# Optimization experiments

Hardware: AMD Instinct MI355X
Metric: run time of the kernel (lower is better)

## Reference

```python
import jax, jax.numpy as jnp
import numpy as np

EPS = 1e-08


def _norm(H, add):
    # Faithful to GTN.norm: transpose, mask/set diagonal, row-normalize by degree, transpose back.
    # The original O(N^3) mm(deg_inv_diag, H) is expressed as an O(N^2) row scaling (same math).
    Ht = H.T
    n = Ht.shape[0]
    eye = jnp.eye(n, dtype=H.dtype)
    Ht = Ht * (1.0 - eye)
    if add:
        Ht = Ht + eye
    deg = jnp.sum(Ht, axis=1)
    deg_inv = jnp.where(deg == 0, 0.0, 1.0 / (deg + EPS))
    return (deg_inv[:, None] * Ht).T


def _gtconv(A, w):
    # A: [E, N, N]; w: [C, E, 1, 1] -> softmax over E, weighted sum of adjacency channels.
    s = jax.nn.softmax(w[:, :, 0, 0], axis=1)  # [C, E]
    return jnp.einsum('ce,eij->cij', s, A)     # [C, N, N]


def setup_inputs() -> dict:
    key = jax.random.key(0)
    k = jax.random.split(key, 6)
    E, N, C, w_in, w_out = 5, 2048, 2, 256, 64
    A = jax.random.uniform(k[0], (E, N, N), dtype=jnp.float32)
    X = jax.random.normal(k[1], (N, w_in), dtype=jnp.float32)
    conv_w_l0_1 = jax.random.normal(k[2], (C, E, 1, 1), dtype=jnp.float32)
    conv_w_l0_2 = jax.random.normal(k[3], (C, E, 1, 1), dtype=jnp.float32)
    conv_w_l1 = jax.random.normal(k[4], (C, E, 1, 1), dtype=jnp.float32)
    gcn_weight = jax.random.normal(k[5], (w_in, w_out), dtype=jnp.float32) * (1.0 / np.sqrt(w_in))
    return {"A": A, "X": X, "conv_w_l0_1": conv_w_l0_1, "conv_w_l0_2": conv_w_l0_2,
            "conv_w_l1": conv_w_l1, "gcn_weight": gcn_weight}


def reference(A, X, conv_w_l0_1, conv_w_l0_2, conv_w_l1, gcn_weight):
    N = A.shape[1]
    # Layer 0 (first=True): two GTConvs, meta-path composition via bmm.
    a = _gtconv(A, conv_w_l0_1)            # [C, N, N]
    b = _gtconv(A, conv_w_l0_2)            # [C, N, N]
    H = jnp.einsum('cij,cjk->cik', a, b)   # [C, N, N]
    # Layer 1 (first=False): normalize per channel, then compose with new conv.
    H = jax.vmap(lambda h: _norm(h, False))(H)
    a1 = _gtconv(A, conv_w_l1)
    H = jnp.einsum('cij,cjk->cik', H, a1)
    # GCN readout per channel: mm(norm_add(H_c).T, X @ W), relu, concat along features.
    Xw = X @ gcn_weight                     # [N, w_out]
    Hn = jax.vmap(lambda h: _norm(h, True))(H)   # [C, N, N]
    Xc = jax.nn.relu(jnp.einsum('cji,jk->cik', Hn, Xw))  # [C, N, w_out]
    X_ = jnp.transpose(Xc, (1, 0, 2)).reshape(N, -1)     # [N, C*w_out]
    return X_
```

## Files before the change

kernel.cpp:

```cpp
#include <hip/hip_runtime.h>
#include <cstdint>
#include <cstddef>

typedef unsigned short u16;
typedef __attribute__((ext_vector_type(8))) short short8;
typedef __attribute__((ext_vector_type(4))) float v4f;

static constexpr size_t NN = (size_t)2048 * 2048;
#define N2 2048

typedef __attribute__((address_space(1))) const unsigned int guint;
typedef __attribute__((address_space(3))) unsigned int luint;

__device__ __forceinline__ float b2f_bits(uint32_t hi) { union { uint32_t u; float f; } v; v.u = hi; return v.f; }
__device__ __forceinline__ float b2f(u16 x) { return b2f_bits((uint32_t)x << 16); }
__device__ __forceinline__ u16 f2b(float f) {
  union { float f; uint32_t u; } v; v.f = f;
  uint32_t r = v.u + 0x7fffu + ((v.u >> 16) & 1u);
  return (u16)(r >> 16);
}
__device__ __forceinline__ uint4 pack8(const float* f) {
  uint4 u;
  u.x = (uint32_t)f2b(f[0]) | ((uint32_t)f2b(f[1]) << 16);
  u.y = (uint32_t)f2b(f[2]) | ((uint32_t)f2b(f[3]) << 16);
  u.z = (uint32_t)f2b(f[4]) | ((uint32_t)f2b(f[5]) << 16);
  u.w = (uint32_t)f2b(f[6]) | ((uint32_t)f2b(f[7]) << 16);
  return u;
}
__device__ __forceinline__ void unp8(uint4 u, float* f) {
  f[0] = b2f_bits(u.x << 16); f[1] = b2f_bits(u.x & 0xffff0000u);
  f[2] = b2f_bits(u.y << 16); f[3] = b2f_bits(u.y & 0xffff0000u);
  f[4] = b2f_bits(u.z << 16); f[5] = b2f_bits(u.z & 0xffff0000u);
  f[6] = b2f_bits(u.w << 16); f[7] = b2f_bits(u.w & 0xffff0000u);
}
__device__ __forceinline__ float sgprf(float x) {
  union { float f; int i; } v; v.f = x;
  v.i = __builtin_amdgcn_readfirstlane(v.i);
  return v.f;
}

__global__ __launch_bounds__(512, 2) void conv_kernel(
    const float* __restrict__ A, const float* __restrict__ w1,
    const float* __restrict__ w2, const float* __restrict__ w3,
    const float* __restrict__ X, const float* __restrict__ W,
    u16* __restrict__ abf, u16* __restrict__ bbt, u16* __restrict__ a1t,
    u16* __restrict__ a1r, u16* __restrict__ Xwt)
{
  __shared__ u16 LT[4][64 * 64];
  const int t = threadIdx.x;
  const int i0 = blockIdx.y * 64, j0 = blockIdx.x * 64;
  const int m = t >> 3;
  const int cg = t & 7;
  const int n0 = cg * 8;

  float sc[3][2][5];
  {
    const float* wsrc[3] = { w1, w2, w3 };
    for (int q = 0; q < 3; ++q)
      for (int c = 0; c < 2; ++c) {
        float v[5], mx = -1e30f, sum = 0.f;
        #pragma unroll
        for (int e = 0; e < 5; ++e) { v[e] = wsrc[q][c * 5 + e]; mx = fmaxf(mx, v[e]); }
        #pragma unroll
        for (int e = 0; e < 5; ++e) { v[e] = expf(v[e] - mx); sum += v[e]; }
        #pragma unroll
        for (int e = 0; e < 5; ++e) sc[q][c][e] = sgprf(v[e] / sum);
      }
  }

  float av[2][8], bv[2][8], cv[2][8];
  #pragma unroll
  for (int c = 0; c < 2; ++c)
    #pragma unroll
    for (int u = 0; u < 8; ++u) { av[c][u] = 0.f; bv[c][u] = 0.f; cv[c][u] = 0.f; }

  #pragma unroll
  for (int e = 0; e < 5; ++e) {
    const float* base = A + (size_t)e * NN + (size_t)(i0 + m) * N2 + (j0 + n0);
    float4 x0 = ((const float4*)base)[0];
    float4 x1 = ((const float4*)base)[1];
    float f[8] = { x0.x, x0.y, x0.z, x0.w, x1.x, x1.y, x1.z, x1.w };
    #pragma unroll
    for (int c = 0; c < 2; ++c)
      #pragma unroll
      for (int u = 0; u < 8; ++u) {
        av[c][u] += sc[0][c][e] * f[u];
        bv[c][u] += sc[1][c][e] * f[u];
        cv[c][u] += sc[2][c][e] * f[u];
      }
  }

  #pragma unroll
  for (int c = 0; c < 2; ++c) {
    *(uint4*)(abf + (size_t)c * NN + (size_t)(i0 + m) * N2 + (j0 + n0)) = pack8(av[c]);
    *(uint4*)(a1r + (size_t)c * NN + (size_t)(i0 + m) * N2 + (j0 + n0)) = pack8(cv[c]);
  }
  const int swb = ((m >> 3) ^ cg) & 7;
  const int mlo = m & 7;
  #pragma unroll
  for (int c = 0; c < 2; ++c)
    #pragma unroll
    for (int u = 0; u < 8; ++u) {
      const int idx = (n0 + u) * 64 + swb * 8 + mlo;
      LT[c][idx]     = f2b(bv[c][u]);
      LT[2 + c][idx] = f2b(cv[c][u]);
    }
  __syncthreads();
  {
    const int on = t >> 3;
    const int mb = t & 7;
    const int src = on * 64 + (((mb ^ (on >> 3)) & 7) * 8);
    #pragma unroll
    for (int c = 0; c < 2; ++c) {
      *(uint4*)(bbt + (size_t)c * NN + (size_t)(j0 + on) * N2 + (i0 + mb * 8)) =
          *(const uint4*)&LT[c][src];
      *(uint4*)(a1t + (size_t)c * NN + (size_t)(j0 + on) * N2 + (i0 + mb * 8)) =
          *(const uint4*)&LT[2 + c][src];
    }
  }
  if (blockIdx.y < 8) {
    const int n = (int)(blockIdx.y * 32 + blockIdx.x) * 8 + (t >> 6);
    const int k = t & 63;
    float acc = 0.f;
    for (int mm = 0; mm < 256; ++mm)
      acc += X[n * 256 + mm] * W[mm * 64 + k];
    Xwt[(size_t)k * N2 + n] = f2b(acc);
  }
}

template<bool TOUT>
__global__ __launch_bounds__(256, 3) void gemm_kernel(
    const u16* __restrict__ Ain, const u16* __restrict__ Btin,
    u16* __restrict__ Cout, float* __restrict__ csp, float* __restrict__ diag)
{
  const int c = blockIdx.z;
  const u16* Ac = Ain + (size_t)c * NN;
  const u16* Bc = Btin + (size_t)c * NN;
  const int m0 = blockIdx.y * 128, n0 = blockIdx.x * 128;
  const int t = threadIdx.x, w = t >> 6, lane = t & 63;
  const int quad = lane >> 4, r = lane & 15;
  __shared__ u16 SM[128 * 64 + 128 * 64];
  u16* As = SM;
  u16* Bs = SM + 128 * 64;

  v4f zero4 = { 0.f, 0.f, 0.f, 0.f };
  v4f acc[2][8];
  #pragma unroll
  for (int i = 0; i < 2; ++i)
    #pragma unroll
    for (int j = 0; j < 8; ++j) acc[i][j] = zero4;

  const int srow = lane >> 3;
  const int sgran = (lane & 7) ^ srow;

  for (int kt = 0; kt < 2048; kt += 64) {
    __syncthreads();
    #pragma unroll
    for (int i = 0; i < 4; ++i) {
      const int chunk = i * 4 + w;
      const u16* ga = Ac + (size_t)(m0 + chunk * 8 + srow) * N2 + kt + sgran * 8;
      __builtin_amdgcn_global_load_lds((guint*)ga, (luint*)(As + chunk * 512), 16, 0, 0);
    }
    #pragma unroll
    for (int i = 0; i < 4; ++i) {
      const int chunk = i * 4 + w;
      const u16* gb = Bc + (size_t)(n0 + chunk * 8 + srow) * N2 + kt + sgran * 8;
      __builtin_amdgcn_global_load_lds((guint*)gb, (luint*)(Bs + chunk * 512), 16, 0, 0);
    }
    __syncthreads();
    #pragma unroll
    for (int ks = 0; ks < 2; ++ks) {
      const int sl = ((ks * 4 + quad) ^ (r & 7)) * 8;
      short8 af[2], bf[8];
      #pragma unroll
      for (int i = 0; i < 2; ++i)
        af[i] = *(const short8*)(As + (w * 32 + i * 16 + r) * 64 + sl);
      #pragma unroll
      for (int j = 0; j < 8; ++j)
        bf[j] = *(const short8*)(Bs + (j * 16 + r) * 64 + sl);
      #pragma unroll
      for (int i = 0; i < 2; ++i)
        #pragma unroll
        for (int j = 0; j < 8; ++j)
          acc[i][j] = __builtin_amdgcn_mfma_f32_16x16x32_bf16(af[i], bf[j], acc[i][j], 0, 0, 0);
    }
  }
  if (blockIdx.x == blockIdx.y) {
    #pragma unroll
    for (int i = 0; i < 2; ++i) {
      const int rowg = m0 + w * 32 + i * 16 + quad * 4;
      #pragma unroll
      for (int j = 0; j < 8; ++j) {
        const int colg = n0 + j * 16 + r;
        #pragma unroll
        for (int g = 0; g < 4; ++g)
          if (rowg + g == colg) diag[c * N2 + colg] = acc[i][j][g];
      }
    }
  }
  if constexpr (!TOUT) {
    u16* Cc = Cout + (size_t)c * NN;
    #pragma unroll
    for (int i = 0; i < 2; ++i) {
      const int rowg = m0 + w * 32 + i * 16 + quad * 4;
      #pragma unroll
      for (int j = 0; j < 8; ++j) {
        const int colg = n0 + j * 16 + r;
        #pragma unroll
        for (int g = 0; g < 4; ++g)
          Cc[(size_t)(rowg + g) * N2 + colg] = f2b(acc[i][j][g]);
      }
    }
  }
  float s[8];
  #pragma unroll
  for (int j = 0; j < 8; ++j) {
    s[j] = 0.f;
    #pragma unroll
    for (int i = 0; i < 2; ++i)
      #pragma unroll
      for (int g = 0; g < 4; ++g) s[j] += acc[i][j][g];
    s[j] += __shfl_xor(s[j], 16);
    s[j] += __shfl_xor(s[j], 32);
  }
  __syncthreads();
  float* csl = (float*)SM;
  if (quad == 0) {
    #pragma unroll
    for (int j = 0; j < 8; ++j) csl[w * 128 + j * 16 + r] = s[j];
  }
  __syncthreads();
  if (t < 128) {
    const float v = csl[t] + csl[128 + t] + csl[256 + t] + csl[384 + t];
    csp[((size_t)(c * 16) + blockIdx.y) * N2 + n0 + t] = v;
  }
  if constexpr (TOUT) {
    u16* tb = SM;
    u16* Cc = Cout + (size_t)c * NN;
    #pragma unroll
    for (int h = 0; h < 2; ++h) {
      __syncthreads();
      #pragma unroll
      for (int i = 0; i < 2; ++i) {
        #pragma unroll
        for (int jl = 0; jl < 4; ++jl) {
          const int j = h * 4 + jl;
          #pragma unroll
          for (int g = 0; g < 4; ++g)
            tb[(jl * 16 + r) * 136 + (w * 32 + i * 16 + quad * 4 + g)] = f2b(acc[i][j][g]);
        }
      }
      __syncthreads();
      const int rown = t >> 2, seg = t & 3;
      const u16* ps = tb + rown * 136 + seg * 32;
      uint4* pd = (uint4*)(Cc + (size_t)(n0 + h * 64 + rown) * N2 + m0 + seg * 32);
      pd[0] = ((const uint4*)ps)[0];
      pd[1] = ((const uint4*)ps)[1];
      pd[2] = ((const uint4*)ps)[2];
      pd[3] = ((const uint4*)ps)[3];
    }
  }
}

__global__ __launch_bounds__(256) void zgemm_kernel(
    const u16* __restrict__ Ht, const u16* __restrict__ Xwt, float* __restrict__ Zp,
    const float* __restrict__ csp, const float* __restrict__ diag,
    float* __restrict__ ci, float* __restrict__ wv)
{
  const int c = blockIdx.z, split = blockIdx.y;
  const int m0 = blockIdx.x * 128;
  const u16* Ac = Ht + (size_t)c * NN;
  const int t = threadIdx.x, w = t >> 6, lane = t & 63;
  const int quad = lane >> 4, r = lane & 15;
  __shared__ u16 As[128 * 64];
  __shared__ u16 Bs[64 * 64];

  v4f zero4 = { 0.f, 0.f, 0.f, 0.f };
  v4f acc[2][4];
  #pragma unroll
  for (int i = 0; i < 2; ++i)
    #pragma unroll
    for (int j = 0; j < 4; ++j) acc[i][j] = zero4;

  const int srow = lane >> 3;
  const int sgran = (lane & 7) ^ srow;

  for (int kk = 0; kk < 4; ++kk) {
    const int kt = split * 256 + kk * 64;
    __syncthreads();
    #pragma unroll
    for (int i = 0; i < 4; ++i) {
      const int chunk = i * 4 + w;
      const u16* ga = Ac + (size_t)(m0 + chunk * 8 + srow) * N2 + kt + sgran * 8;
      __builtin_amdgcn_global_load_lds((guint*)ga, (luint*)(As + chunk * 512), 16, 0, 0);
    }
    #pragma unroll
    for (int i = 0; i < 2; ++i) {
      const int chunk = i * 4 + w;
      const u16* gb = Xwt + (size_t)(chunk * 8 + srow) * N2 + kt + sgran * 8;
      __builtin_amdgcn_global_load_lds((guint*)gb, (luint*)(Bs + chunk * 512), 16, 0, 0);
    }
    __syncthreads();
    #pragma unroll
    for (int ks = 0; ks < 2; ++ks) {
      const int sl = ((ks * 4 + quad) ^ (r & 7)) * 8;
      short8 af[2], bf[4];
      #pragma unroll
      for (int i = 0; i < 2; ++i)
        af[i] = *(const short8*)(As + (w * 32 + i * 16 + r) * 64 + sl);
      #pragma unroll
      for (int j = 0; j < 4; ++j)
        bf[j] = *(const short8*)(Bs + (j * 16 + r) * 64 + sl);
      #pragma unroll
      for (int i = 0; i < 2; ++i)
        #pragma unroll
        for (int j = 0; j < 4; ++j)
          acc[i][j] = __builtin_amdgcn_mfma_f32_16x16x32_bf16(af[i], bf[j], acc[i][j], 0, 0, 0);
    }
  }
  const size_t pbase = (size_t)(split * 2 + c) * 64;
  #pragma unroll
  for (int i = 0; i < 2; ++i) {
    const int rowg = m0 + w * 32 + i * 16 + quad * 4;
    #pragma unroll
    for (int j = 0; j < 4; ++j) {
      const int colg = j * 16 + r;
      *(v4f*)(Zp + (pbase + colg) * (size_t)N2 + rowg) = acc[i][j];
    }
  }
  if (blockIdx.x == 0 && blockIdx.y == 0) {
    for (int q = t; q < 2048; q += 256) {
      float cs = 0.f;
      #pragma unroll
      for (int s = 0; s < 16; ++s) cs += csp[((size_t)(c * 16) + s) * N2 + q];
      const float deg = cs - diag[c * N2 + q];
      const float v = (deg == 0.f) ? 0.f : 1.f / (deg + 1e-8f);
      ci[c * N2 + q] = v;
      wv[c * N2 + q] = v * deg;
    }
  }
}

__global__ __launch_bounds__(256) void dcol_kernel(
    const u16* __restrict__ Ht, const u16* __restrict__ a1r,
    const float* __restrict__ ci, const float* __restrict__ wv,
    float* __restrict__ dp, float* __restrict__ cp)
{
  const int qg = blockIdx.x, c = blockIdx.y;
  const int p0 = threadIdx.x * 8;
  float dacc[8] = {0,0,0,0,0,0,0,0};
  float cacc[8] = {0,0,0,0,0,0,0,0};
  const u16* hb = Ht  + (size_t)c * NN + (size_t)(qg * 16) * N2 + p0;
  const u16* ab = a1r + (size_t)c * NN + (size_t)(qg * 16) * N2 + p0;
  for (int qq = 0; qq < 16; ++qq) {
    const int q = qg * 16 + qq;
    const float cq = ci[c * N2 + q];
    const float wq = wv[c * N2 + q];
    uint4 hu = *(const uint4*)(hb + (size_t)qq * N2);
    uint4 au = *(const uint4*)(ab + (size_t)qq * N2);
    float h[8], a[8];
    unp8(hu, h); unp8(au, a);
    #pragma unroll
    for (int u = 0; u < 8; ++u) {
      cacc[u] += wq * a[u];
      const float tv = cq * h[u] * a[u];
      dacc[u] += (p0 + u == q) ? 0.f : tv;
    }
  }
  float* dd = dp + (size_t)(c * 128 + qg) * N2 + p0;
  float* cd = cp + (size_t)(c * 128 + qg) * N2 + p0;
  v4f d0 = { dacc[0], dacc[1], dacc[2], dacc[3] };
  v4f d1 = { dacc[4], dacc[5], dacc[6], dacc[7] };
  v4f c0 = { cacc[0], cacc[1], cacc[2], cacc[3] };
  v4f c1 = { cacc[4], cacc[5], cacc[6], cacc[7] };
  *(v4f*)dd = d0; *(v4f*)(dd + 4) = d1;
  *(v4f*)cd = c0; *(v4f*)(cd + 4) = c1;
}

__global__ __launch_bounds__(256) void yfix_kernel(
    const float* __restrict__ Zp, const float* __restrict__ ci,
    const float* __restrict__ diag1, const u16* __restrict__ Xwt,
    u16* __restrict__ Yt)
{
  const int idx = blockIdx.x * 256 + threadIdx.x;
  const int i = idx & 2047, k = (idx >> 11) & 63, c = idx >> 17;
  float z = 0.f;
  #pragma unroll
  for (int s = 0; s < 8; ++s)
    z += Zp[(size_t)((s * 2 + c) * 64 + k) * N2 + i];
  const float xw = b2f(Xwt[(size_t)k * N2 + i]);
  const float y = ci[c * N2 + i] * (z - diag1[c * N2 + i] * xw);
  Yt[(size_t)c * 64 * N2 + (size_t)k * N2 + i] = f2b(y);
}

__global__ void fin_kernel(const float* __restrict__ dp, const float* __restrict__ cp,
                           float* __restrict__ diag2, float* __restrict__ dinv2)
{
  const int idx = blockIdx.x * 256 + threadIdx.x;
  const int c = idx >> 11, i = idx & 2047;
  float ds = 0.f, cs = 0.f;
  for (int b = 0; b < 128; ++b) {
    ds += dp[(size_t)(c * 128 + b) * N2 + i];
    cs += cp[(size_t)(c * 128 + b) * N2 + i];
  }
  const float deg = cs - ds + 1.0f;
  diag2[idx] = ds;
  dinv2[idx] = (deg == 0.f) ? 0.f : 1.f / (deg + 1e-8f);
}

__global__ __launch_bounds__(256) void tgemm_kernel(
    const u16* __restrict__ a1t, const u16* __restrict__ Yt, float* __restrict__ Tp)
{
  const int c = blockIdx.z, split = blockIdx.y;
  const int m0 = blockIdx.x * 128;
  const u16* Ac = a1t + (size_t)c * NN;
  const u16* Bc = Yt + (size_t)c * (64 * (size_t)N2);
  const int t = threadIdx.x, w = t >> 6, lane = t & 63;
  const int quad = lane >> 4, r = lane & 15;
  __shared__ u16 As[128 * 64];
  __shared__ u16 Bs[64 * 64];

  v4f zero4 = { 0.f, 0.f, 0.f, 0.f };
  v4f acc[2][4];
  #pragma unroll
  for (int i = 0; i < 2; ++i)
    #pragma unroll
    for (int j = 0; j < 4; ++j) acc[i][j] = zero4;

  const int srow = lane >> 3;
  const int sgran = (lane & 7) ^ srow;

  for (int kk = 0; kk < 4; ++kk) {
    const int kt = split * 256 + kk * 64;
    __syncthreads();
    #pragma unroll
    for (int i = 0; i < 4; ++i) {
      const int chunk = i * 4 + w;
      const u16* ga = Ac + (size_t)(m0 + chunk * 8 + srow) * N2 + kt + sgran * 8;
      __builtin_amdgcn_global_load_lds((guint*)ga, (luint*)(As + chunk * 512), 16, 0, 0);
    }
    #pragma unroll
    for (int i = 0; i < 2; ++i) {
      const int chunk = i * 4 + w;
      const u16* gb = Bc + (size_t)(chunk * 8 + srow) * N2 + kt + sgran * 8;
      __builtin_amdgcn_global_load_lds((guint*)gb, (luint*)(Bs + chunk * 512), 16, 0, 0);
    }
    __syncthreads();
    #pragma unroll
    for (int ks = 0; ks < 2; ++ks) {
      const int sl = ((ks * 4 + quad) ^ (r & 7)) * 8;
      short8 af[2], bf[4];
      #pragma unroll
      for (int i = 0; i < 2; ++i)
        af[i] = *(const short8*)(As + (w * 32 + i * 16 + r) * 64 + sl);
      #pragma unroll
      for (int j = 0; j < 4; ++j)
        bf[j] = *(const short8*)(Bs + (j * 16 + r) * 64 + sl);
      #pragma unroll
      for (int i = 0; i < 2; ++i)
        #pragma unroll
        for (int j = 0; j < 4; ++j)
          acc[i][j] = __builtin_amdgcn_mfma_f32_16x16x32_bf16(af[i], bf[j], acc[i][j], 0, 0, 0);
    }
  }
  const size_t pbase = (size_t)(split * 2 + c) * 2048;
  #pragma unroll
  for (int i = 0; i < 2; ++i) {
    const int rowg = m0 + w * 32 + i * 16 + quad * 4;
    #pragma unroll
    for (int j = 0; j < 4; ++j) {
      const int colg = j * 16 + r;
      #pragma unroll
      for (int g = 0; g < 4; ++g)
        Tp[(pbase + rowg + g) * 64 + colg] = acc[i][j][g];
    }
  }
}

__global__ void epilogue_kernel(const float* __restrict__ Tp, const float* __restrict__ diag2,
                                const float* __restrict__ dinv2, const u16* __restrict__ Xwt,
                                float* __restrict__ out)
{
  const int idx = blockIdx.x * 256 + threadIdx.x;
  const int k = idx & 63;
  const int c = (idx >> 6) & 1;
  const int i = idx >> 7;
  float T = 0.f;
  #pragma unroll
  for (int s = 0; s < 8; ++s)
    T += Tp[((size_t)(s * 2 + c) * 2048 + i) * 64 + k];
  const float hd = diag2[c * N2 + i];
  const float dv = dinv2[c * N2 + i];
  const float xw = b2f(Xwt[(size_t)k * N2 + i]);
  float v = dv * (T - hd * xw + xw);
  v = v > 0.f ? v : 0.f;
  out[(size_t)i * 128 + c * 64 + k] = v;
}

extern "C" void kernel_launch(void* const* d_in, const int* in_sizes, int n_in,
                              void* d_out, int out_size, void* d_ws, size_t ws_size,
                              hipStream_t stream) {
  const float* A  = (const float*)d_in[0];
  const float* X  = (const float*)d_in[1];
  const float* w1 = (const float*)d_in[2];
  const float* w2 = (const float*)d_in[3];
  const float* w3 = (const float*)d_in[4];
  const float* W  = (const float*)d_in[5];
  float* out = (float*)d_out;
  char* ws = (char*)d_ws;

  u16*   abf   = (u16*)(ws + 0);
  u16*   bbt   = (u16*)(ws + 16777216);
  u16*   a1t   = (u16*)(ws + 33554432);
  u16*   a1r   = (u16*)(ws + 50331648);
  u16*   Ht    = (u16*)(ws + 67108864);
  u16*   Xwt   = (u16*)(ws + 83886080);
  float* cspa  = (float*)(ws + 84148224);
  float* diag1 = (float*)(ws + 84410368);
  float* ci1   = (float*)(ws + 84426752);
  float* w2v   = (float*)(ws + 84443136);
  float* diag2 = (float*)(ws + 84459520);
  float* dinv2 = (float*)(ws + 84475904);
  float* Zp    = (float*)(ws + 0);
  float* dp    = (float*)(ws + 16777216);
  float* cp    = (float*)(ws + 18874368);
  u16*   Yt    = (u16*)(ws + 20971520);
  float* Tp    = (float*)(ws + 50331648);

  conv_kernel<<<dim3(32, 32), 512, 0, stream>>>(A, w1, w2, w3, X, W, abf, bbt, a1t, a1r, Xwt);
  gemm_kernel<true><<<dim3(16, 16, 2), 256, 0, stream>>>(abf, bbt, Ht, cspa, diag1);
  zgemm_kernel<<<dim3(16, 8, 2), 256, 0, stream>>>(Ht, Xwt, Zp, cspa, diag1, ci1, w2v);
  dcol_kernel<<<dim3(128, 2), 256, 0, stream>>>(Ht, a1r, ci1, w2v, dp, cp);
  yfix_kernel<<<1024, 256, 0, stream>>>(Zp, ci1, diag1, Xwt, Yt);
  fin_kernel<<<16, 256, 0, stream>>>(dp, cp, diag2, dinv2);
  tgemm_kernel<<<dim3(16, 8, 2), 256, 0, stream>>>(a1t, Yt, Tp);
  epilogue_kernel<<<1024, 256, 0, stream>>>(Tp, diag2, dinv2, Xwt, out);
}
```

Measured before the change: 246.4 us.

## Double split-K parallelism, fold fin into yfix, shrink conv LDS

```diff
diff --git a/kernel.cpp b/kernel.cpp
--- a/kernel.cpp
+++ b/kernel.cpp
@@ -46,7 +46,7 @@
     u16* __restrict__ abf, u16* __restrict__ bbt, u16* __restrict__ a1t,
     u16* __restrict__ a1r, u16* __restrict__ Xwt)
 {
-  __shared__ u16 LT[4][64 * 64];
+  __shared__ u16 LT[2][64 * 64];
   const int t = threadIdx.x;
   const int i0 = blockIdx.y * 64, j0 = blockIdx.x * 64;
   const int m = t >> 3;
@@ -97,26 +97,23 @@
   }
   const int swb = ((m >> 3) ^ cg) & 7;
   const int mlo = m & 7;
-  #pragma unroll
-  for (int c = 0; c < 2; ++c)
+  const int on = t >> 3;
+  const int mb = t & 7;
+  const int src = on * 64 + (((mb ^ (on >> 3)) & 7) * 8);
+  #pragma unroll
+  for (int c = 0; c < 2; ++c) {
+    if (c == 1) __syncthreads();
     #pragma unroll
     for (int u = 0; u < 8; ++u) {
       const int idx = (n0 + u) * 64 + swb * 8 + mlo;
-      LT[c][idx]     = f2b(bv[c][u]);
-      LT[2 + c][idx] = f2b(cv[c][u]);
-    }
-  __syncthreads();
-  {
-    const int on = t >> 3;
-    const int mb = t & 7;
-    const int src = on * 64 + (((mb ^ (on >> 3)) & 7) * 8);
-    #pragma unroll
-    for (int c = 0; c < 2; ++c) {
-      *(uint4*)(bbt + (size_t)c * NN + (size_t)(j0 + on) * N2 + (i0 + mb * 8)) =
-          *(const uint4*)&LT[c][src];
-      *(uint4*)(a1t + (size_t)c * NN + (size_t)(j0 + on) * N2 + (i0 + mb * 8)) =
-          *(const uint4*)&LT[2 + c][src];
-    }
+      LT[0][idx] = f2b(bv[c][u]);
+      LT[1][idx] = f2b(cv[c][u]);
+    }
+    __syncthreads();
+    *(uint4*)(bbt + (size_t)c * NN + (size_t)(j0 + on) * N2 + (i0 + mb * 8)) =
+        *(const uint4*)&LT[0][src];
+    *(uint4*)(a1t + (size_t)c * NN + (size_t)(j0 + on) * N2 + (i0 + mb * 8)) =
+        *(const uint4*)&LT[1][src];
   }
   if (blockIdx.y < 8) {
     const int n = (int)(blockIdx.y * 32 + blockIdx.x) * 8 + (t >> 6);
@@ -128,7 +125,6 @@
   }
 }
 
-template<bool TOUT>
 __global__ __launch_bounds__(256, 3) void gemm_kernel(
     const u16* __restrict__ Ain, const u16* __restrict__ Btin,
     u16* __restrict__ Cout, float* __restrict__ csp, float* __restrict__ diag)
@@ -198,20 +194,6 @@
       }
     }
   }
-  if constexpr (!TOUT) {
-    u16* Cc = Cout + (size_t)c * NN;
-    #pragma unroll
-    for (int i = 0; i < 2; ++i) {
-      const int rowg = m0 + w * 32 + i * 16 + quad * 4;
-      #pragma unroll
-      for (int j = 0; j < 8; ++j) {
-        const int colg = n0 + j * 16 + r;
-        #pragma unroll
-        for (int g = 0; g < 4; ++g)
-          Cc[(size_t)(rowg + g) * N2 + colg] = f2b(acc[i][j][g]);
-      }
-    }
-  }
   float s[8];
   #pragma unroll
   for (int j = 0; j < 8; ++j) {
@@ -234,7 +216,7 @@
     const float v = csl[t] + csl[128 + t] + csl[256 + t] + csl[384 + t];
     csp[((size_t)(c * 16) + blockIdx.y) * N2 + n0 + t] = v;
   }
-  if constexpr (TOUT) {
+  {
     u16* tb = SM;
     u16* Cc = Cout + (size_t)c * NN;
     #pragma unroll
@@ -262,7 +244,7 @@
   }
 }
 
-__global__ __launch_bounds__(256) void zgemm_kernel(
+__global__ __launch_bounds__(256, 2) void zgemm_kernel(
     const u16* __restrict__ Ht, const u16* __restrict__ Xwt, float* __restrict__ Zp,
     const float* __restrict__ csp, const float* __restrict__ diag,
     float* __restrict__ ci, float* __restrict__ wv)
@@ -285,8 +267,9 @@
   const int srow = lane >> 3;
   const int sgran = (lane & 7) ^ srow;
 
-  for (int kk = 0; kk < 4; ++kk) {
-    const int kt = split * 256 + kk * 64;
+  #pragma unroll
+  for (int kk = 0; kk < 2; ++kk) {
+    const int kt = split * 128 + kk * 64;
     __syncthreads();
     #pragma unroll
     for (int i = 0; i < 4; ++i) {
@@ -341,7 +324,7 @@
   }
 }
 
-__global__ __launch_bounds__(256) void dcol_kernel(
+__global__ __launch_bounds__(256, 2) void dcol_kernel(
     const u16* __restrict__ Ht, const u16* __restrict__ a1r,
     const float* __restrict__ ci, const float* __restrict__ wv,
     float* __restrict__ dp, float* __restrict__ cp)
@@ -350,10 +333,10 @@
   const int p0 = threadIdx.x * 8;
   float dacc[8] = {0,0,0,0,0,0,0,0};
   float cacc[8] = {0,0,0,0,0,0,0,0};
-  const u16* hb = Ht  + (size_t)c * NN + (size_t)(qg * 16) * N2 + p0;
-  const u16* ab = a1r + (size_t)c * NN + (size_t)(qg * 16) * N2 + p0;
-  for (int qq = 0; qq < 16; ++qq) {
-    const int q = qg * 16 + qq;
+  const u16* hb = Ht  + (size_t)c * NN + (size_t)(qg * 8) * N2 + p0;
+  const u16* ab = a1r + (size_t)c * NN + (size_t)(qg * 8) * N2 + p0;
+  for (int qq = 0; qq < 8; ++qq) {
+    const int q = qg * 8 + qq;
     const float cq = ci[c * N2 + q];
     const float wq = wv[c * N2 + q];
     uint4 hu = *(const uint4*)(hb + (size_t)qq * N2);
@@ -367,8 +350,8 @@
       dacc[u] += (p0 + u == q) ? 0.f : tv;
     }
   }
-  float* dd = dp + (size_t)(c * 128 + qg) * N2 + p0;
-  float* cd = cp + (size_t)(c * 128 + qg) * N2 + p0;
+  float* dd = dp + (size_t)(c * 256 + qg) * N2 + p0;
+  float* cd = cp + (size_t)(c * 256 + qg) * N2 + p0;
   v4f d0 = { dacc[0], dacc[1], dacc[2], dacc[3] };
   v4f d1 = { dacc[4], dacc[5], dacc[6], dacc[7] };
   v4f c0 = { cacc[0], cacc[1], cacc[2], cacc[3] };
@@ -380,35 +363,34 @@
 __global__ __launch_bounds__(256) void yfix_kernel(
     const float* __restrict__ Zp, const float* __restrict__ ci,
     const float* __restrict__ diag1, const u16* __restrict__ Xwt,
-    u16* __restrict__ Yt)
+    u16* __restrict__ Yt, const float* __restrict__ dp,
+    const float* __restrict__ cp, float* __restrict__ diag2,
+    float* __restrict__ dinv2)
 {
   const int idx = blockIdx.x * 256 + threadIdx.x;
   const int i = idx & 2047, k = (idx >> 11) & 63, c = idx >> 17;
   float z = 0.f;
   #pragma unroll
-  for (int s = 0; s < 8; ++s)
+  for (int s = 0; s < 16; ++s)
     z += Zp[(size_t)((s * 2 + c) * 64 + k) * N2 + i];
   const float xw = b2f(Xwt[(size_t)k * N2 + i]);
   const float y = ci[c * N2 + i] * (z - diag1[c * N2 + i] * xw);
   Yt[(size_t)c * 64 * N2 + (size_t)k * N2 + i] = f2b(y);
-}
-
-__global__ void fin_kernel(const float* __restrict__ dp, const float* __restrict__ cp,
-                           float* __restrict__ diag2, float* __restrict__ dinv2)
-{
-  const int idx = blockIdx.x * 256 + threadIdx.x;
-  const int c = idx >> 11, i = idx & 2047;
-  float ds = 0.f, cs = 0.f;
-  for (int b = 0; b < 128; ++b) {
-    ds += dp[(size_t)(c * 128 + b) * N2 + i];
-    cs += cp[(size_t)(c * 128 + b) * N2 + i];
-  }
-  const float deg = cs - ds + 1.0f;
-  diag2[idx] = ds;
-  dinv2[idx] = (deg == 0.f) ? 0.f : 1.f / (deg + 1e-8f);
-}
-
-__global__ __launch_bounds__(256) void tgemm_kernel(
+  if (blockIdx.x < 16) {
+    const int idx2 = blockIdx.x * 256 + threadIdx.x;
+    const int c2 = idx2 >> 11, i2 = idx2 & 2047;
+    float ds = 0.f, cs = 0.f;
+    for (int b = 0; b < 256; ++b) {
+      ds += dp[(size_t)(c2 * 256 + b) * N2 + i2];
+      cs += cp[(size_t)(c2 * 256 + b) * N2 + i2];
+    }
+    const float deg = cs - ds + 1.0f;
+    diag2[idx2] = ds;
+    dinv2[idx2] = (deg == 0.f) ? 0.f : 1.f / (deg + 1e-8f);
+  }
+}
+
+__global__ __launch_bounds__(256, 2) void tgemm_kernel(
     const u16* __restrict__ a1t, const u16* __restrict__ Yt, float* __restrict__ Tp)
 {
   const int c = blockIdx.z, split = blockIdx.y;
@@ -430,8 +412,9 @@
   const int srow = lane >> 3;
   const int sgran = (lane & 7) ^ srow;
 
-  for (int kk = 0; kk < 4; ++kk) {
-    const int kt = split * 256 + kk * 64;
+  #pragma unroll
+  for (int kk = 0; kk < 2; ++kk) {
+    const int kt = split * 128 + kk * 64;
     __syncthreads();
     #pragma unroll
     for (int i = 0; i < 4; ++i) {
@@ -487,7 +470,7 @@
   const int i = idx >> 7;
   float T = 0.f;
   #pragma unroll
-  for (int s = 0; s < 8; ++s)
+  for (int s = 0; s < 16; ++s)
     T += Tp[((size_t)(s * 2 + c) * 2048 + i) * 64 + k];
   const float hd = diag2[c * N2 + i];
   const float dv = dinv2[c * N2 + i];
@@ -523,16 +506,15 @@
   float* dinv2 = (float*)(ws + 84475904);
   float* Zp    = (float*)(ws + 0);
   float* dp    = (float*)(ws + 16777216);
-  float* cp    = (float*)(ws + 18874368);
-  u16*   Yt    = (u16*)(ws + 20971520);
+  float* cp    = (float*)(ws + 20971520);
+  u16*   Yt    = (u16*)(ws + 25165824);
   float* Tp    = (float*)(ws + 50331648);
 
   conv_kernel<<<dim3(32, 32), 512, 0, stream>>>(A, w1, w2, w3, X, W, abf, bbt, a1t, a1r, Xwt);
-  gemm_kernel<true><<<dim3(16, 16, 2), 256, 0, stream>>>(abf, bbt, Ht, cspa, diag1);
-  zgemm_kernel<<<dim3(16, 8, 2), 256, 0, stream>>>(Ht, Xwt, Zp, cspa, diag1, ci1, w2v);
-  dcol_kernel<<<dim3(128, 2), 256, 0, stream>>>(Ht, a1r, ci1, w2v, dp, cp);
-  yfix_kernel<<<1024, 256, 0, stream>>>(Zp, ci1, diag1, Xwt, Yt);
-  fin_kernel<<<16, 256, 0, stream>>>(dp, cp, diag2, dinv2);
-  tgemm_kernel<<<dim3(16, 8, 2), 256, 0, stream>>>(a1t, Yt, Tp);
+  gemm_kernel<<<dim3(16, 16, 2), 256, 0, stream>>>(abf, bbt, Ht, cspa, diag1);
+  zgemm_kernel<<<dim3(16, 16, 2), 256, 0, stream>>>(Ht, Xwt, Zp, cspa, diag1, ci1, w2v);
+  dcol_kernel<<<dim3(256, 2), 256, 0, stream>>>(Ht, a1r, ci1, w2v, dp, cp);
+  yfix_kernel<<<1024, 256, 0, stream>>>(Zp, ci1, diag1, Xwt, Yt, dp, cp, diag2, dinv2);
+  tgemm_kernel<<<dim3(16, 16, 2), 256, 0, stream>>>(a1t, Yt, Tp);
   epilogue_kernel<<<1024, 256, 0, stream>>>(Tp, diag2, dinv2, Xwt, out);
 }
```

After: 245.8 us. Within noise of the previous version (-0.2%).
